# Kernel optimization log

Hardware: AMD Instinct MI355X
Metric: run time of the kernel (lower is better)

The kernel has to match this reference:

```python
import math
import jax, jax.numpy as jnp
import numpy as np

B, T, D, H, FACTOR = 8, 4096, 1024, 16, 5
DH = D // H


def setup_inputs() -> dict:
    key = jax.random.key(0)
    ks = jax.random.split(key, 7)
    u = max(1, min(int(FACTOR * math.log(T + 1)), T))  # = 41
    s = 1.0 / np.sqrt(D).astype(np.float32)
    x = jax.random.normal(ks[0], (B, T, D), jnp.float32)
    Wq = jax.random.normal(ks[1], (D, D), jnp.float32) * s
    Wk = jax.random.normal(ks[2], (D, D), jnp.float32) * s
    Wv = jax.random.normal(ks[3], (D, D), jnp.float32) * s
    Wo = jax.random.normal(ks[4], (D, D), jnp.float32) * s
    bo = jax.random.normal(ks[5], (D,), jnp.float32) * 0.01
    # unique indices, mirroring torch.randperm(T)[:u]
    idx = jax.random.permutation(ks[6], T)[:u].astype(jnp.int32)
    return {"x": x, "Wq": Wq, "Wk": Wk, "Wv": Wv, "Wo": Wo, "bo": bo, "idx": idx}


def reference(x, Wq, Wk, Wv, Wo, bo, idx):
    Bx, Tx, Dx = x.shape
    scale = 1.0 / np.sqrt(DH).astype(np.float32)

    def proj(W):  # torch Linear: x @ W.T, then split heads -> [B,H,T,Dh]
        return (x @ W.T).reshape(Bx, Tx, H, DH).transpose(0, 2, 1, 3)

    Q = proj(Wq)
    K = proj(Wk)
    V = proj(Wv)

    Qs = Q[:, :, idx, :]                                   # [B,H,u,Dh] gather
    scores = jnp.einsum('bhud,bhtd->bhut', Qs, K) * scale  # [B,H,u,T]
    attn = jax.nn.softmax(scores, axis=-1)
    ctx = jnp.einsum('bhut,bhtd->bhud', attn, V)           # [B,H,u,Dh]

    # mean over the u sampled positions fills non-sampled slots
    out = jnp.broadcast_to(ctx.mean(axis=2, keepdims=True), (Bx, H, Tx, DH))
    out = out.at[:, :, idx, :].set(ctx)                    # scatter ctx back

    y = out.transpose(0, 2, 1, 3).reshape(Bx, Tx, Dx)
    return y @ Wo.T + bo
```

## Files before the change

kernel.cpp:

```cpp
#include <hip/hip_runtime.h>
#include <hip/hip_bf16.h>

#define B_  8
#define T_  4096
#define D_  1024
#define H_  16
#define DH_ 64
#define NC_ 4

typedef __bf16 bf8 __attribute__((ext_vector_type(8)));
typedef float f32x4 __attribute__((ext_vector_type(4)));

__device__ __forceinline__ unsigned short f2bf_rn(float f) {
    unsigned u = __float_as_uint(f);
    unsigned r = (u + 0x7FFF + ((u >> 16) & 1)) >> 16;
    return (unsigned short)r;
}

__device__ __forceinline__ void async_load16(const void* gp, void* lp) {
    __builtin_amdgcn_global_load_lds(
        (const __attribute__((address_space(1))) unsigned*)(gp),
        (__attribute__((address_space(3))) unsigned*)(lp), 16, 0, 0);
}


__global__ void k_sel(const int* __restrict__ idx, int* __restrict__ sel, int U) {
    for (int t = threadIdx.x; t < T_; t += 256) sel[t] = 0;
    __syncthreads();
    if (threadIdx.x < U) sel[idx[threadIdx.x]] = threadIdx.x + 1;
}

__global__ void k_gather(const float* __restrict__ x, const int* __restrict__ idx,
                         float* __restrict__ xs, int U) {
    int bi = blockIdx.x;
    int b = bi / U, i = bi - b * U;
    int t = idx[i];
    const float4* src = (const float4*)(x + ((size_t)(b * T_ + t)) * D_);
    float4* dst = (float4*)(xs + (size_t)bi * D_);
    dst[threadIdx.x] = src[threadIdx.x];
}

__global__ void k_cvt_flat(const float* __restrict__ src, short* __restrict__ dst) {
    size_t i = ((size_t)blockIdx.x * 256 + threadIdx.x) * 8;
    float4 a = *(const float4*)(src + i);
    float4 b = *(const float4*)(src + i + 4);
    short4 s0, s1;
    s0.x = (short)f2bf_rn(a.x); s0.y = (short)f2bf_rn(a.y);
    s0.z = (short)f2bf_rn(a.z); s0.w = (short)f2bf_rn(a.w);
    s1.x = (short)f2bf_rn(b.x); s1.y = (short)f2bf_rn(b.y);
    s1.z = (short)f2bf_rn(b.z); s1.w = (short)f2bf_rn(b.w);
    *(short4*)(dst + i) = s0;
    *(short4*)(dst + i + 4) = s1;
}

__global__ void k_zpad(short* __restrict__ Qtb, int HU, int MP) {
    int bi = blockIdx.x;
    int npad = MP - HU;
    int b = bi / npad, r = bi - b * npad;
    short4 z = {0, 0, 0, 0};
    *(short4*)(Qtb + ((size_t)b * MP + HU + r) * D_ + threadIdx.x * 4) = z;
}

__global__ __launch_bounds__(256) void k_proj(const float* __restrict__ A,
                                              const float* __restrict__ W,
                                              const float* __restrict__ bias,
                                              float* __restrict__ C, int M) {
    __shared__ float As[32][64 + 4];
    __shared__ float Bs[32][64 + 4];
    int m0 = blockIdx.x * 64, n0 = blockIdx.y * 64;
    int tid = threadIdx.x;
    int lr = tid >> 3;
    int lc = (tid & 7) * 4;
    int ty = tid >> 4, tx = tid & 15;
    float acc[4][4] = {{0.f}};
    for (int k0 = 0; k0 < D_; k0 += 32) {
#pragma unroll
        for (int half = 0; half < 2; ++half) {
            int r = lr + half * 32;
            int gm = m0 + r;
            float4 v = make_float4(0.f, 0.f, 0.f, 0.f);
            if (gm < M) v = *(const float4*)(A + (size_t)gm * D_ + k0 + lc);
            As[lc + 0][r] = v.x; As[lc + 1][r] = v.y; As[lc + 2][r] = v.z; As[lc + 3][r] = v.w;
            int gn = n0 + r;
            float4 w = *(const float4*)(W + (size_t)gn * D_ + k0 + lc);
            Bs[lc + 0][r] = w.x; Bs[lc + 1][r] = w.y; Bs[lc + 2][r] = w.z; Bs[lc + 3][r] = w.w;
        }
        __syncthreads();
#pragma unroll
        for (int kk = 0; kk < 32; ++kk) {
            float4 a = *(const float4*)&As[kk][ty * 4];
            float4 bb = *(const float4*)&Bs[kk][tx * 4];
            acc[0][0] += a.x * bb.x; acc[0][1] += a.x * bb.y; acc[0][2] += a.x * bb.z; acc[0][3] += a.x * bb.w;
            acc[1][0] += a.y * bb.x; acc[1][1] += a.y * bb.y; acc[1][2] += a.y * bb.z; acc[1][3] += a.y * bb.w;
            acc[2][0] += a.z * bb.x; acc[2][1] += a.z * bb.y; acc[2][2] += a.z * bb.z; acc[2][3] += a.z * bb.w;
            acc[3][0] += a.w * bb.x; acc[3][1] += a.w * bb.y; acc[3][2] += a.w * bb.z; acc[3][3] += a.w * bb.w;
        }
        __syncthreads();
    }
#pragma unroll
    for (int i = 0; i < 4; ++i) {
        int gm = m0 + ty * 4 + i;
        if (gm < M) {
            int gn = n0 + tx * 4;
            float4 v = make_float4(acc[i][0], acc[i][1], acc[i][2], acc[i][3]);
            if (bias) {
                v.x += bias[gn + 0]; v.y += bias[gn + 1];
                v.z += bias[gn + 2]; v.w += bias[gn + 3];
            }
            *(float4*)(C + (size_t)gm * D_ + gn) = v;
        }
    }
}

__global__ __launch_bounds__(256) void k_qth(const float* __restrict__ Qs,
                                             const float* __restrict__ Wk,
                                             short* __restrict__ Qtb, int U, int MP) {
    __shared__ float As[32][64 + 4];
    __shared__ float Bs[32][64 + 4];
    int h = blockIdx.z;
    int m0 = blockIdx.x * 64, n0 = blockIdx.y * 64;
    int BU = B_ * U;
    int tid = threadIdx.x;
    int lr = tid >> 3, lc = (tid & 7) * 4;
    int ty = tid >> 4, tx = tid & 15;
    float acc[4][4] = {{0.f}};
    for (int k0 = 0; k0 < DH_; k0 += 32) {
#pragma unroll
        for (int half = 0; half < 2; ++half) {
            int r = lr + half * 32;
            int gm = m0 + r;
            float4 v = make_float4(0.f, 0.f, 0.f, 0.f);
            if (gm < BU) v = *(const float4*)(Qs + (size_t)gm * D_ + h * DH_ + k0 + lc);
            As[lc + 0][r] = v.x; As[lc + 1][r] = v.y; As[lc + 2][r] = v.z; As[lc + 3][r] = v.w;
            int kr = (tid >> 4) + half * 16;
            int nc = (tid & 15) * 4;
            float4 w = *(const float4*)(Wk + ((size_t)(h * DH_ + k0 + kr)) * D_ + n0 + nc);
            *(float4*)&Bs[kr][nc] = w;
        }
        __syncthreads();
#pragma unroll
        for (int kk = 0; kk < 32; ++kk) {
            float4 a = *(const float4*)&As[kk][ty * 4];
            float4 bb = *(const float4*)&Bs[kk][tx * 4];
            acc[0][0] += a.x * bb.x; acc[0][1] += a.x * bb.y; acc[0][2] += a.x * bb.z; acc[0][3] += a.x * bb.w;
            acc[1][0] += a.y * bb.x; acc[1][1] += a.y * bb.y; acc[1][2] += a.y * bb.z; acc[1][3] += a.y * bb.w;
            acc[2][0] += a.z * bb.x; acc[2][1] += a.z * bb.y; acc[2][2] += a.z * bb.z; acc[2][3] += a.z * bb.w;
            acc[3][0] += a.w * bb.x; acc[3][1] += a.w * bb.y; acc[3][2] += a.w * bb.z; acc[3][3] += a.w * bb.w;
        }
        __syncthreads();
    }
#pragma unroll
    for (int i = 0; i < 4; ++i) {
        int gm = m0 + ty * 4 + i;
        if (gm < BU) {
            int b = gm / U, ii = gm - b * U;
            short4 s;
            s.x = (short)f2bf_rn(0.125f * acc[i][0]);
            s.y = (short)f2bf_rn(0.125f * acc[i][1]);
            s.z = (short)f2bf_rn(0.125f * acc[i][2]);
            s.w = (short)f2bf_rn(0.125f * acc[i][3]);
            *(short4*)(Qtb + ((size_t)b * MP + h * U + ii) * D_ + n0 + tx * 4) = s;
        }
    }
}

#define GEMM_NT 16

__device__ __forceinline__ void stage64(const short* __restrict__ Ag,
                                        const short* __restrict__ Bg,
                                        short* lA, short* lB, int kt, int tid) {
#pragma unroll
    for (int i = 0; i < 4; ++i) {
        int li = i * 512 + tid;
        int row = li >> 3, sl = li & 7;
        int off = row * D_ + kt + ((sl ^ (row & 7)) << 3);
        async_load16(Ag + off, lA + li * 8);
        async_load16(Bg + off, lB + li * 8);
    }
}

__device__ __forceinline__ bf8 lds_frag(const short* l, int R, int slot) {
    return *(const bf8*)(l + R * 64 + (((slot) ^ (R & 7)) << 3));
}

__device__ __forceinline__ void gemm256_core(const short* __restrict__ Ag,
                                             const short* __restrict__ Bg,
                                             short* lA0, short* lB0,
                                             f32x4 (&acc)[8][4]) {
    int tid = threadIdx.x;
    int lane = tid & 63, w = tid >> 6;
    int wr = w >> 2, wc = w & 3;
    int ln = lane & 15, q = lane >> 4;
#pragma unroll
    for (int mi = 0; mi < 8; ++mi)
#pragma unroll
        for (int ni = 0; ni < 4; ++ni)
            acc[mi][ni] = (f32x4){0.f, 0.f, 0.f, 0.f};

    stage64(Ag, Bg, lA0, lB0, 0, tid);
    stage64(Ag, Bg, lA0 + 16384, lB0 + 16384, 64, tid);

#pragma unroll 1
    for (int t = 0; t < GEMM_NT; ++t) {
        const int p = t & 1;
        short* lA = lA0 + p * 16384;
        short* lB = lB0 + p * 16384;
        if (t < GEMM_NT - 1) asm volatile("s_waitcnt vmcnt(8)" ::: "memory");
        else                 asm volatile("s_waitcnt vmcnt(0)" ::: "memory");
        __builtin_amdgcn_s_barrier();

        bf8 bfrag[4][2], afrag[4][2];
#pragma unroll
        for (int ni = 0; ni < 4; ++ni)
#pragma unroll
            for (int kh = 0; kh < 2; ++kh)
                bfrag[ni][kh] = lds_frag(lB, wc * 64 + ni * 16 + ln, kh * 4 + q);
#pragma unroll
        for (int mi = 0; mi < 4; ++mi)
#pragma unroll
            for (int kh = 0; kh < 2; ++kh)
                afrag[mi][kh] = lds_frag(lA, wr * 128 + mi * 16 + ln, kh * 4 + q);
        __builtin_amdgcn_s_setprio(1);
#pragma unroll
        for (int kh = 0; kh < 2; ++kh)
#pragma unroll
            for (int mi = 0; mi < 4; ++mi)
#pragma unroll
                for (int ni = 0; ni < 4; ++ni)
                    acc[mi][ni] = __builtin_amdgcn_mfma_f32_16x16x32_bf16(
                        afrag[mi][kh], bfrag[ni][kh], acc[mi][ni], 0, 0, 0);
        __builtin_amdgcn_s_setprio(0);
#pragma unroll
        for (int mi = 0; mi < 4; ++mi)
#pragma unroll
            for (int kh = 0; kh < 2; ++kh)
                afrag[mi][kh] = lds_frag(lA, wr * 128 + 64 + mi * 16 + ln, kh * 4 + q);
        __builtin_amdgcn_s_setprio(1);
#pragma unroll
        for (int kh = 0; kh < 2; ++kh)
#pragma unroll
            for (int mi = 0; mi < 4; ++mi)
#pragma unroll
                for (int ni = 0; ni < 4; ++ni)
                    acc[4 + mi][ni] = __builtin_amdgcn_mfma_f32_16x16x32_bf16(
                        afrag[mi][kh], bfrag[ni][kh], acc[4 + mi][ni], 0, 0, 0);
        __builtin_amdgcn_s_setprio(0);
        asm volatile("" ::: "memory");
        __builtin_amdgcn_s_barrier();
        if (t + 2 < GEMM_NT)
            stage64(Ag, Bg, lA, lB, (t + 2) * 64, tid);
    }
}

__global__ __launch_bounds__(512, 2) void k_scores2(const short* __restrict__ Qtb,
                                                    const short* __restrict__ xb,
                                                    short* __restrict__ attnb, int MP) {
    __shared__ short lA[2][16384];
    __shared__ short lB[2][16384];
    int bid = blockIdx.x;
    int lg = (bid & 7) * (gridDim.x >> 3) + (bid >> 3);
    int MT = MP >> 8;
    int per_b = MT << 4;
    int b = lg / per_b;
    int r = lg - b * per_b;
    int mt = r >> 4, nt = r & 15;
    const short* Ag = Qtb + ((size_t)b * MP + mt * 256) * D_;
    const short* Bg = xb + ((size_t)b * T_ + nt * 256) * D_;
    f32x4 acc[8][4];
    gemm256_core(Ag, Bg, &lA[0][0], &lB[0][0], acc);

    short* Cb = attnb + (size_t)b * MP * T_;
    int tid = threadIdx.x;
    int lane = tid & 63, w = tid >> 6;
    int wr = w >> 2, wc = w & 3;
    int ln = lane & 15, q = lane >> 4;
    int row0 = mt * 256 + wr * 128;
    int col0 = nt * 256 + wc * 64;
#pragma unroll
    for (int mi = 0; mi < 8; ++mi)
#pragma unroll
        for (int ni = 0; ni < 4; ++ni) {
            int col = col0 + ni * 16 + ln;
#pragma unroll
            for (int rr = 0; rr < 4; ++rr) {
                int grow = row0 + mi * 16 + q * 4 + rr;
                Cb[(size_t)grow * T_ + col] = (short)f2bf_rn(__expf(acc[mi][ni][rr]));
            }
        }
}

__global__ __launch_bounds__(512, 2) void k_v2(const short* __restrict__ xb,
                                               const short* __restrict__ Wvb,
                                               short* __restrict__ Vt) {
    __shared__ short lA[2][16384];
    __shared__ short lB[2][16384];
    int bid = blockIdx.x;
    int lg = (bid & 7) * (gridDim.x >> 3) + (bid >> 3);
    int mt = lg >> 2, nt = lg & 3;
    const short* Ag = xb + (size_t)mt * 256 * D_;
    const short* Bg = Wvb + (size_t)nt * 256 * D_;
    f32x4 acc[8][4];
    gemm256_core(Ag, Bg, &lA[0][0], &lB[0][0], acc);

    int tid = threadIdx.x;
    int lane = tid & 63, w = tid >> 6;
    int wr = w >> 2, wc = w & 3;
    int ln = lane & 15, q = lane >> 4;
    int h = nt * 4 + wc;
    int b = mt >> 4;
    int tIn = (mt & 15) * 256 + wr * 128;
    const int PITCH = 136;
    short* ep = &lA[0][0] + w * 2304;
    size_t vbase = ((size_t)(b * H_ + h) * DH_) * T_;
#pragma unroll
    for (int ni = 0; ni < 4; ++ni) {
#pragma unroll
        for (int mi = 0; mi < 8; ++mi) {
            short4 s;
            s.x = (short)f2bf_rn(acc[mi][ni][0]);
            s.y = (short)f2bf_rn(acc[mi][ni][1]);
            s.z = (short)f2bf_rn(acc[mi][ni][2]);
            s.w = (short)f2bf_rn(acc[mi][ni][3]);
            *(short4*)(ep + ln * PITCH + mi * 16 + q * 4) = s;
        }
        __syncthreads();
#pragma unroll
        for (int it = 0; it < 2; ++it) {
            int dhl = it * 8 + (lane >> 3);
            int seg = lane & 7;
            bf8 v0 = *(const bf8*)(ep + dhl * PITCH + seg * 8);
            bf8 v1 = *(const bf8*)(ep + dhl * PITCH + (seg + 8) * 8);
            int dh = ni * 16 + dhl;
            *(bf8*)(Vt + vbase + (size_t)dh * T_ + tIn + seg * 8) = v0;
            *(bf8*)(Vt + vbase + (size_t)dh * T_ + tIn + 64 + seg * 8) = v1;
        }
        __syncthreads();
    }
}

__global__ __launch_bounds__(256) void k_pv(const short* __restrict__ attnb,
                                            const short* __restrict__ Vt,
                                            float* __restrict__ Op,
                                            float* __restrict__ rsp,
                                            int U, int MP) {
    __shared__ short vt[64 * 136];
    int gid = blockIdx.x;
    int c = gid & (NC_ - 1);
    int bh = gid >> 2;
    int h = bh & (H_ - 1);
    int b = bh >> 4;
    int tid = threadIdx.x;
    int lane = tid & 63, w = tid >> 6;
    int quad = lane >> 4;
    const short* Arow = attnb + ((size_t)b * MP + h * U) * T_;
    const short* Vrow = Vt + (size_t)bh * DH_ * T_;

    f32x4 O[3];
#pragma unroll
    for (int mi = 0; mi < 3; ++mi) O[mi] = (f32x4){0.f, 0.f, 0.f, 0.f};
    float rs[3] = {0.f, 0.f, 0.f};

    for (int tt = 0; tt < (T_ / NC_) / 128; ++tt) {
        int t0 = c * (T_ / NC_) + tt * 128;
#pragma unroll
        for (int it = 0; it < 4; ++it) {
            int idx = it * 256 + tid;
            int dh = idx >> 4, seg = idx & 15;
            bf8 v = *(const bf8*)(Vrow + (size_t)dh * T_ + t0 + seg * 8);
            *(bf8*)(vt + dh * 136 + seg * 8) = v;
        }
        __syncthreads();
        bf8 af[3][4];
#pragma unroll
        for (int mi = 0; mi < 3; ++mi)
#pragma unroll
            for (int kf = 0; kf < 4; ++kf)
                af[mi][kf] = *(const bf8*)(Arow + (size_t)(mi * 16 + (lane & 15)) * T_ + t0 + kf * 32 + quad * 8);
        if (w == 0) {
#pragma unroll
            for (int mi = 0; mi < 3; ++mi)
#pragma unroll
                for (int kf = 0; kf < 4; ++kf)
#pragma unroll
                    for (int j = 0; j < 8; ++j) rs[mi] += (float)af[mi][kf][j];
        }
#pragma unroll
        for (int kf = 0; kf < 4; ++kf) {
            bf8 bfr = *(const bf8*)(vt + (w * 16 + (lane & 15)) * 136 + kf * 32 + quad * 8);
#pragma unroll
            for (int mi = 0; mi < 3; ++mi)
                O[mi] = __builtin_amdgcn_mfma_f32_16x16x32_bf16(af[mi][kf], bfr, O[mi], 0, 0, 0);
        }
        __syncthreads();
    }
#pragma unroll
    for (int mi = 0; mi < 3; ++mi)
#pragma unroll
        for (int r = 0; r < 4; ++r)
            Op[((size_t)gid * 48 + mi * 16 + quad * 4 + r) * DH_ + w * 16 + (lane & 15)] = O[mi][r];
    if (w == 0) {
#pragma unroll
        for (int mi = 0; mi < 3; ++mi) {
            rs[mi] += __shfl_xor(rs[mi], 16);
            rs[mi] += __shfl_xor(rs[mi], 32);
            if (quad == 0) rsp[(size_t)gid * 48 + mi * 16 + lane] = rs[mi];
        }
    }
}

__global__ __launch_bounds__(256) void k_rows2(const float* __restrict__ Op,
                                               const float* __restrict__ rsp,
                                               float* __restrict__ R, int U) {
    __shared__ float inv[48];
    __shared__ float msum[4][64];
    int bh = blockIdx.x;
    int b = bh >> 4, h = bh & (H_ - 1);
    int tid = threadIdx.x;
    if (tid < 48) {
        float s = 0.f;
        for (int cc = 0; cc < NC_; ++cc) s += rsp[(size_t)(bh * NC_ + cc) * 48 + tid];
        inv[tid] = 1.f / s;
    }
    __syncthreads();
    int dh = tid & 63, ig = tid >> 6;
    float acc = 0.f;
    for (int p = 0; p < 11; ++p) {
        int i = p * 4 + ig;
        if (i < U) {
            float o = 0.f;
            for (int cc = 0; cc < NC_; ++cc)
                o += Op[((size_t)(bh * NC_ + cc) * 48 + i) * DH_ + dh];
            float v = o * inv[i];
            R[((size_t)b * (U + 1) + 1 + i) * D_ + h * DH_ + dh] = v;
            acc += v;
        }
    }
    msum[ig][dh] = acc;
    __syncthreads();
    if (ig == 0)
        R[((size_t)b * (U + 1)) * D_ + h * DH_ + dh] =
            (msum[0][dh] + msum[1][dh] + msum[2][dh] + msum[3][dh]) / (float)U;
}

__global__ __launch_bounds__(256) void k_fill(const float* __restrict__ Yr,
                                              const int* __restrict__ sel,
                                              float* __restrict__ y, int U) {
    int blk = blockIdx.x;
    int b = blk >> 12, t = blk & (T_ - 1);
    int j = sel[t];
    const float4* src = (const float4*)(Yr + ((size_t)b * (U + 1) + j) * D_);
    float4* dst = (float4*)(y + (size_t)blk * D_);
    dst[threadIdx.x] = src[threadIdx.x];
}

extern "C" void kernel_launch(void* const* d_in, const int* in_sizes, int n_in,
                              void* d_out, int out_size, void* d_ws, size_t ws_size,
                              hipStream_t stream) {
    const float* x  = (const float*)d_in[0];
    const float* Wq = (const float*)d_in[1];
    const float* Wk = (const float*)d_in[2];
    const float* Wv = (const float*)d_in[3];
    const float* Wo = (const float*)d_in[4];
    const float* bo = (const float*)d_in[5];
    const int*  idx = (const int*)d_in[6];
    int U = in_sizes[6];
    int HU = H_ * U;
    int MP = ((HU + 127) / 128) * 128;

    char* w = (char*)d_ws;
    auto alloc = [&](size_t bytes) { char* p = w; w += (bytes + 255) & ~(size_t)255; return p; };

    float* xs    = (float*)alloc((size_t)B_ * U * D_ * 4);
    float* Qs    = (float*)alloc((size_t)B_ * U * D_ * 4);
    short* Qtb   = (short*)alloc((size_t)B_ * MP * D_ * 2);
    short* xb    = (short*)alloc((size_t)B_ * T_ * D_ * 2);
    short* Wvb   = (short*)alloc((size_t)D_ * D_ * 2);
    short* attnb = (short*)alloc((size_t)B_ * MP * T_ * 2);
    short* Vtb   = (short*)alloc((size_t)B_ * D_ * T_ * 2);
    float* Opb   = (float*)alloc((size_t)B_ * H_ * NC_ * 48 * DH_ * 4);
    float* rspb  = (float*)alloc((size_t)B_ * H_ * NC_ * 48 * 4);
    float* R     = (float*)alloc((size_t)B_ * (U + 1) * D_ * 4);
    float* Yr    = (float*)alloc((size_t)B_ * (U + 1) * D_ * 4);
    int*   sel   = (int*)alloc((size_t)T_ * 4);

    int MT = MP / 256;

    k_sel<<<dim3(1), dim3(256), 0, stream>>>(idx, sel, U);
    k_gather<<<dim3(B_ * U), dim3(256), 0, stream>>>(x, idx, xs, U);
    k_proj<<<dim3((B_ * U + 63) / 64, D_ / 64), dim3(256), 0, stream>>>(xs, Wq, nullptr, Qs, B_ * U);
    k_cvt_flat<<<dim3((size_t)B_ * T_ * D_ / 2048), dim3(256), 0, stream>>>(x, xb);
    k_cvt_flat<<<dim3((size_t)D_ * D_ / 2048), dim3(256), 0, stream>>>(Wv, Wvb);
    k_zpad<<<dim3(B_ * (MP - HU)), dim3(256), 0, stream>>>(Qtb, HU, MP);
    k_qth<<<dim3((B_ * U + 63) / 64, D_ / 64, H_), dim3(256), 0, stream>>>(Qs, Wk, Qtb, U, MP);
    k_scores2<<<dim3(B_ * MT * 16), dim3(512), 0, stream>>>(Qtb, xb, attnb, MP);
    k_v2<<<dim3((B_ * T_ / 256) * (D_ / 256)), dim3(512), 0, stream>>>(xb, Wvb, Vtb);
    k_pv<<<dim3(B_ * H_ * NC_), dim3(256), 0, stream>>>(attnb, Vtb, Opb, rspb, U, MP);
    k_rows2<<<dim3(B_ * H_), dim3(256), 0, stream>>>(Opb, rspb, R, U);
    k_proj<<<dim3((B_ * (U + 1) + 63) / 64, D_ / 64), dim3(256), 0, stream>>>(R, Wo, bo, Yr, B_ * (U + 1));
    k_fill<<<dim3(B_ * T_), dim3(256), 0, stream>>>(Yr, sel, (float*)d_out, U);
}
```

Measured before the change: 587.9 us.

## Restructure GEMM core into phased pipeline with k-major LDS layout

Replaces the two-stage double-buffered GEMM main loop with a four-phase schedule per K-tile. Each phase loads a fragment set from LDS, issues an async global-to-LDS copy of one quarter of the next tile, then runs 16 MFMAs, with barriers between phases. The LDS layout becomes k-slot-major (no XOR swizzle), so fragment reads are contiguous. The aim is to interleave global loads, LDS reads and MFMA work more finely, at the cost of many more barriers per iteration, a prefetch distance of one tile instead of two, and possible LDS bank conflicts without the swizzle. A sync is added before the V epilogue reuses LDS.

Result: slower. 620.2 us (+5.5%).

```diff
diff --git a/kernel.cpp b/kernel.cpp
--- a/kernel.cpp
+++ b/kernel.cpp
@@ -166,90 +166,117 @@
 
 #define GEMM_NT 16
 
-__device__ __forceinline__ void stage64(const short* __restrict__ Ag,
-                                        const short* __restrict__ Bg,
-                                        short* lA, short* lB, int kt, int tid) {
-#pragma unroll
-    for (int i = 0; i < 4; ++i) {
-        int li = i * 512 + tid;
-        int row = li >> 3, sl = li & 7;
-        int off = row * D_ + kt + ((sl ^ (row & 7)) << 3);
-        async_load16(Ag + off, lA + li * 8);
-        async_load16(Bg + off, lB + li * 8);
-    }
-}
-
-__device__ __forceinline__ bf8 lds_frag(const short* l, int R, int slot) {
-    return *(const bf8*)(l + R * 64 + (((slot) ^ (R & 7)) << 3));
-}
-
-__device__ __forceinline__ void gemm256_core(const short* __restrict__ Ag,
-                                             const short* __restrict__ Bg,
-                                             short* lA0, short* lB0,
-                                             f32x4 (&acc)[8][4]) {
-    int tid = threadIdx.x;
-    int lane = tid & 63, w = tid >> 6;
-    int wr = w >> 2, wc = w & 3;
-    int ln = lane & 15, q = lane >> 4;
+__device__ __forceinline__ void gemm256_8ph(const short* __restrict__ Ag,
+                                            const short* __restrict__ Bg,
+                                            short* __restrict__ lA0,
+                                            short* __restrict__ lB0,
+                                            f32x4 (&acc)[8][4]) {
+    const int tid = threadIdx.x;
+    const int lane = tid & 63, w = tid >> 6;
+    const int wr = w >> 2, wc = w & 3;
+    const int ln = lane & 15, q = lane >> 4;
 #pragma unroll
     for (int mi = 0; mi < 8; ++mi)
 #pragma unroll
         for (int ni = 0; ni < 4; ++ni)
             acc[mi][ni] = (f32x4){0.f, 0.f, 0.f, 0.f};
 
-    stage64(Ag, Bg, lA0, lB0, 0, tid);
-    stage64(Ag, Bg, lA0 + 16384, lB0 + 16384, 64, tid);
+    const int li0 = tid, li1 = 512 + tid;
+    const size_t ga0 = (size_t)(li0 & 255) * D_ + ((li0 >> 8) << 3);
+    const size_t ga1 = (size_t)(li1 & 255) * D_ + ((li1 >> 8) << 3);
+    const int ld0 = li0 * 8, ld1 = li1 * 8;
+
+#define STAGE(G, l, kcol)                                   \
+    do {                                                    \
+        async_load16((G) + ga0 + (kcol), (l) + ld0);        \
+        async_load16((G) + ga1 + (kcol), (l) + ld1);        \
+    } while (0)
+
+    STAGE(Ag, lA0, 0);
+    STAGE(Bg, lB0, 0);
+    STAGE(Ag, lA0 + 8192, 32);
+    STAGE(Bg, lB0 + 8192, 32);
+    asm volatile("s_waitcnt vmcnt(0)" ::: "memory");
+    __builtin_amdgcn_s_barrier();
+
+    const int aoff = q * 2048 + (wr * 128 + ln) * 8;
+    const int boff = q * 2048 + (wc * 64 + ln) * 8;
 
 #pragma unroll 1
     for (int t = 0; t < GEMM_NT; ++t) {
-        const int p = t & 1;
-        short* lA = lA0 + p * 16384;
-        short* lB = lB0 + p * 16384;
-        if (t < GEMM_NT - 1) asm volatile("s_waitcnt vmcnt(8)" ::: "memory");
-        else                 asm volatile("s_waitcnt vmcnt(0)" ::: "memory");
-        __builtin_amdgcn_s_barrier();
-
-        bf8 bfrag[4][2], afrag[4][2];
-#pragma unroll
-        for (int ni = 0; ni < 4; ++ni)
-#pragma unroll
-            for (int kh = 0; kh < 2; ++kh)
-                bfrag[ni][kh] = lds_frag(lB, wc * 64 + ni * 16 + ln, kh * 4 + q);
+        const int p = t & 1, pn = p ^ 1;
+        const short* pA = lA0 + p * 16384;
+        const short* pB = lB0 + p * 16384;
+        short* nA = lA0 + pn * 16384;
+        short* nB = lB0 + pn * 16384;
+        const int kn = (t + 1) * 64;
+        const bool more = (t + 1 < GEMM_NT);
+        bf8 af[4], bf[4];
+
+#pragma unroll
+        for (int ni = 0; ni < 4; ++ni) bf[ni] = *(const bf8*)(pB + boff + ni * 128);
+#pragma unroll
+        for (int mi = 0; mi < 4; ++mi) af[mi] = *(const bf8*)(pA + aoff + mi * 128);
+        if (more) STAGE(Ag, nA, kn);
+        __builtin_amdgcn_s_barrier();
+        asm volatile("s_waitcnt lgkmcnt(0)" ::: "memory");
+        __builtin_amdgcn_s_setprio(1);
 #pragma unroll
         for (int mi = 0; mi < 4; ++mi)
 #pragma unroll
-            for (int kh = 0; kh < 2; ++kh)
-                afrag[mi][kh] = lds_frag(lA, wr * 128 + mi * 16 + ln, kh * 4 + q);
+            for (int ni = 0; ni < 4; ++ni)
+                acc[mi][ni] = __builtin_amdgcn_mfma_f32_16x16x32_bf16(af[mi], bf[ni], acc[mi][ni], 0, 0, 0);
+        __builtin_amdgcn_s_setprio(0);
+        __builtin_amdgcn_s_barrier();
+
+#pragma unroll
+        for (int mi = 0; mi < 4; ++mi) af[mi] = *(const bf8*)(pA + aoff + 512 + mi * 128);
+        if (more) STAGE(Bg, nB, kn);
+        __builtin_amdgcn_s_barrier();
+        asm volatile("s_waitcnt lgkmcnt(0)" ::: "memory");
         __builtin_amdgcn_s_setprio(1);
 #pragma unroll
-        for (int kh = 0; kh < 2; ++kh)
-#pragma unroll
-            for (int mi = 0; mi < 4; ++mi)
-#pragma unroll
-                for (int ni = 0; ni < 4; ++ni)
-                    acc[mi][ni] = __builtin_amdgcn_mfma_f32_16x16x32_bf16(
-                        afrag[mi][kh], bfrag[ni][kh], acc[mi][ni], 0, 0, 0);
+        for (int mi = 0; mi < 4; ++mi)
+#pragma unroll
+            for (int ni = 0; ni < 4; ++ni)
+                acc[4 + mi][ni] = __builtin_amdgcn_mfma_f32_16x16x32_bf16(af[mi], bf[ni], acc[4 + mi][ni], 0, 0, 0);
         __builtin_amdgcn_s_setprio(0);
+        if (more) asm volatile("s_waitcnt vmcnt(4)" ::: "memory");
+        else      asm volatile("s_waitcnt vmcnt(0)" ::: "memory");
+        __builtin_amdgcn_s_barrier();
+
+#pragma unroll
+        for (int ni = 0; ni < 4; ++ni) bf[ni] = *(const bf8*)(pB + 8192 + boff + ni * 128);
+#pragma unroll
+        for (int mi = 0; mi < 4; ++mi) af[mi] = *(const bf8*)(pA + 8192 + aoff + mi * 128);
+        if (more) STAGE(Ag, nA + 8192, kn + 32);
+        __builtin_amdgcn_s_barrier();
+        asm volatile("s_waitcnt lgkmcnt(0)" ::: "memory");
+        __builtin_amdgcn_s_setprio(1);
 #pragma unroll
         for (int mi = 0; mi < 4; ++mi)
 #pragma unroll
-            for (int kh = 0; kh < 2; ++kh)
-                afrag[mi][kh] = lds_frag(lA, wr * 128 + 64 + mi * 16 + ln, kh * 4 + q);
+            for (int ni = 0; ni < 4; ++ni)
+                acc[mi][ni] = __builtin_amdgcn_mfma_f32_16x16x32_bf16(af[mi], bf[ni], acc[mi][ni], 0, 0, 0);
+        __builtin_amdgcn_s_setprio(0);
+        __builtin_amdgcn_s_barrier();
+
+#pragma unroll
+        for (int mi = 0; mi < 4; ++mi) af[mi] = *(const bf8*)(pA + 8192 + aoff + 512 + mi * 128);
+        if (more) STAGE(Bg, nB + 8192, kn + 32);
+        __builtin_amdgcn_s_barrier();
+        asm volatile("s_waitcnt lgkmcnt(0)" ::: "memory");
         __builtin_amdgcn_s_setprio(1);
 #pragma unroll
-        for (int kh = 0; kh < 2; ++kh)
-#pragma unroll
-            for (int mi = 0; mi < 4; ++mi)
-#pragma unroll
-                for (int ni = 0; ni < 4; ++ni)
-                    acc[4 + mi][ni] = __builtin_amdgcn_mfma_f32_16x16x32_bf16(
-                        afrag[mi][kh], bfrag[ni][kh], acc[4 + mi][ni], 0, 0, 0);
+        for (int mi = 0; mi < 4; ++mi)
+#pragma unroll
+            for (int ni = 0; ni < 4; ++ni)
+                acc[4 + mi][ni] = __builtin_amdgcn_mfma_f32_16x16x32_bf16(af[mi], bf[ni], acc[4 + mi][ni], 0, 0, 0);
         __builtin_amdgcn_s_setprio(0);
-        asm volatile("" ::: "memory");
-        __builtin_amdgcn_s_barrier();
-        if (t + 2 < GEMM_NT)
-            stage64(Ag, Bg, lA, lB, (t + 2) * 64, tid);
-    }
+        asm volatile("s_waitcnt vmcnt(4)" ::: "memory");
+        __builtin_amdgcn_s_barrier();
+    }
+#undef STAGE
 }
 
 __global__ __launch_bounds__(512, 2) void k_scores2(const short* __restrict__ Qtb,
@@ -267,7 +294,7 @@
     const short* Ag = Qtb + ((size_t)b * MP + mt * 256) * D_;
     const short* Bg = xb + ((size_t)b * T_ + nt * 256) * D_;
     f32x4 acc[8][4];
-    gemm256_core(Ag, Bg, &lA[0][0], &lB[0][0], acc);
+    gemm256_8ph(Ag, Bg, &lA[0][0], &lB[0][0], acc);
 
     short* Cb = attnb + (size_t)b * MP * T_;
     int tid = threadIdx.x;
@@ -300,7 +327,7 @@
     const short* Ag = xb + (size_t)mt * 256 * D_;
     const short* Bg = Wvb + (size_t)nt * 256 * D_;
     f32x4 acc[8][4];
-    gemm256_core(Ag, Bg, &lA[0][0], &lB[0][0], acc);
+    gemm256_8ph(Ag, Bg, &lA[0][0], &lB[0][0], acc);
 
     int tid = threadIdx.x;
     int lane = tid & 63, w = tid >> 6;
@@ -312,6 +339,7 @@
     const int PITCH = 136;
     short* ep = &lA[0][0] + w * 2304;
     size_t vbase = ((size_t)(b * H_ + h) * DH_) * T_;
+    __syncthreads();
 #pragma unroll
     for (int ni = 0; ni < 4; ++ni) {
 #pragma unroll
```
